# Kernel optimization log

Measured on AMD Instinct MI355X. Metric: run time of the kernel, lower is better.

Reference implementation:

```python
import jax, jax.numpy as jnp
import numpy as np


def _gcn(x, src, dst, W, b, M):
    # GCNConv: out = D^{-1/2} (A+I) D^{-1/2} X W + b, messages flow src->dst
    xw = x @ W  # [M, D]
    loops = jnp.arange(M)
    s = jnp.concatenate([src, loops])
    d = jnp.concatenate([dst, loops])
    deg = jax.ops.segment_sum(jnp.ones_like(s, x.dtype), d, num_segments=M)
    dinv = jnp.where(deg > 0, jax.lax.rsqrt(jnp.maximum(deg, 1.0)), 0.0)
    norm = dinv[s] * dinv[d]  # [Eg+M]
    return jax.ops.segment_sum(norm[:, None] * xw[s], d, num_segments=M) + b


def _graph_cross_attention(values, k, q, e_src, e_dst, N):
    # gather-dot, segment softmax over destination tokens, scatter-sum of values
    scale = jnp.sqrt(jnp.asarray(k.shape[1], k.dtype))
    dots = (q[e_dst] * k[e_src]).sum(-1) / scale  # [Ea]
    m = jax.ops.segment_max(dots, e_dst, num_segments=N)
    m = jnp.where(jnp.isfinite(m), m, 0.0)
    w = jnp.exp(dots - m[e_dst])
    den = jax.ops.segment_sum(w, e_dst, num_segments=N)
    w = w / jnp.where(den > 0, den, 1.0)[e_dst]
    return jax.ops.segment_sum(w[:, None] * values[e_src], e_dst, num_segments=N)


def reference(token_embeddings, tokens2edges, edge_index, e2t_src, e2t_dst,
              W_gnn, b_gnn, Wk, bk, Wq, bq, Wl, bl, gate_a, gate_b):
    N = token_embeddings.shape[1]
    M = tokens2edges.shape[1]

    def per_sample(t, t2e, ei, es, ed):
        edge_emb = t[t2e]                                  # [M, D] gather
        edge_emb = _gcn(edge_emb, ei[0], ei[1], W_gnn, b_gnn, M)
        k = edge_emb @ Wk + bk                             # [M, 64]
        q = t @ Wq + bq                                    # [N, 64]
        gatt = _graph_cross_attention(edge_emb, k, q, es, ed, N)  # [N, D]
        new = t + jnp.tanh(gate_a) * gatt
        new = new + jnp.tanh(gate_b) * (new @ Wl + bl)
        return new

    return jax.vmap(per_sample)(token_embeddings, tokens2edges, edge_index, e2t_src, e2t_dst)


def setup_inputs() -> dict:
    B, N, M, Eg, Ea, D, DK = 4, 4096, 16384, 65536, 65536, 512, 64
    key = jax.random.key(0)
    ks = jax.random.split(key, 16)
    s = 0.05  # weight scale to keep activations well-conditioned
    return {
        "token_embeddings": jax.random.normal(ks[0], (B, N, D), jnp.float32),
        "tokens2edges": jax.random.randint(ks[1], (B, M), 0, N),
        "edge_index": jax.random.randint(ks[2], (B, 2, Eg), 0, M),
        "e2t_src": jax.random.randint(ks[3], (B, Ea), 0, M),
        "e2t_dst": jax.random.randint(ks[4], (B, Ea), 0, N),
        "W_gnn": jax.random.normal(ks[5], (D, D), jnp.float32) * s,
        "b_gnn": jax.random.normal(ks[6], (D,), jnp.float32) * s,
        "Wk": jax.random.normal(ks[7], (D, DK), jnp.float32) * s,
        "bk": jax.random.normal(ks[8], (DK,), jnp.float32) * s,
        "Wq": jax.random.normal(ks[9], (D, DK), jnp.float32) * s,
        "bq": jax.random.normal(ks[10], (DK,), jnp.float32) * s,
        "Wl": jax.random.normal(ks[11], (D, D), jnp.float32) * s,
        "bl": jax.random.normal(ks[12], (D,), jnp.float32) * s,
        "gate_a": jax.random.normal(ks[13], (1,), jnp.float32),
        "gate_b": jax.random.normal(ks[14], (1,), jnp.float32),
    }
```

## Files before the change

kernel.cpp:

```cpp
#include <hip/hip_runtime.h>
#include <math.h>

#define BB 4
#define NT 4096
#define ME 16384
#define EG 65536
#define EA 65536
#define DD 512
#define DKK 64

using bf16x8 = __attribute__((ext_vector_type(8))) short;
using f32x4  = __attribute__((ext_vector_type(4))) float;

static __device__ __forceinline__ unsigned short f2bf(float f) {
    unsigned u = __float_as_uint(f);
    u += 0x7fffu + ((u >> 16) & 1u);
    return (unsigned short)(u >> 16);
}
static __device__ __forceinline__ float bf2f(unsigned short u) {
    return __uint_as_float((unsigned)u << 16);
}
static __device__ __forceinline__ void acc8(float* a, uint4 v, float s) {
    a[0] += s * __uint_as_float(v.x << 16);
    a[1] += s * __uint_as_float(v.x & 0xffff0000u);
    a[2] += s * __uint_as_float(v.y << 16);
    a[3] += s * __uint_as_float(v.y & 0xffff0000u);
    a[4] += s * __uint_as_float(v.z << 16);
    a[5] += s * __uint_as_float(v.z & 0xffff0000u);
    a[6] += s * __uint_as_float(v.w << 16);
    a[7] += s * __uint_as_float(v.w & 0xffff0000u);
}
static __device__ __forceinline__ uint4 pack8(const float* a) {
    uint4 o;
    o.x = (unsigned)f2bf(a[0]) | ((unsigned)f2bf(a[1]) << 16);
    o.y = (unsigned)f2bf(a[2]) | ((unsigned)f2bf(a[3]) << 16);
    o.z = (unsigned)f2bf(a[4]) | ((unsigned)f2bf(a[5]) << 16);
    o.w = (unsigned)f2bf(a[6]) | ((unsigned)f2bf(a[7]) << 16);
    return o;
}

#define PREP_GEMM  8
#define PREP_CAST  (PREP_GEMM + 8192)
#define PREP_TRA   (PREP_CAST + 1024)
#define PREP_WQ    (PREP_TRA + 128)
#define PREP_WLT   (PREP_WQ + 1024)
#define PREP_BIAS  (PREP_WLT + 67)
#define PREP_HIST  (PREP_BIAS + 2048)
__global__ __launch_bounds__(256) void k_prep(
    const float* __restrict__ Wgnn, const float* __restrict__ Wk,
    const float* __restrict__ Wq, const float* __restrict__ Wl,
    const float* __restrict__ bgnn, const float* __restrict__ bk,
    const float* __restrict__ bq, const float* __restrict__ t_all,
    const int* __restrict__ ei_all, const int* __restrict__ ed_all,
    unsigned short* __restrict__ BtT, unsigned short* __restrict__ Wlt,
    float* __restrict__ biasG, float* __restrict__ bias640,
    unsigned short* __restrict__ tb, int* __restrict__ cntG, int* __restrict__ cntA)
{
    __shared__ float smem[2048];
    int bx = blockIdx.x, tid = threadIdx.x;
    if (bx < PREP_GEMM) {
        float (*As)[64] = (float(*)[64])smem;
        float (*Bs)[64] = (float(*)[64])(smem + 1024);
        int tx = tid & 15, ty = tid >> 4;
        int bm = bx * 64;
        float acc[4][4] = {};
        long aoff = (long)(bm + (tid >> 2)) * DD;
        int kk0 = (tid & 3) * 4;
        int arowl = tid >> 2;
        for (int k0 = 0; k0 < DD; k0 += 16) {
            float4 av = *(const float4*)(Wgnn + aoff + k0 + kk0);
            As[kk0 + 0][arowl] = av.x;
            As[kk0 + 1][arowl] = av.y;
            As[kk0 + 2][arowl] = av.z;
            As[kk0 + 3][arowl] = av.w;
            float4 bv = *(const float4*)(Wk + (long)(k0 + ty) * 64 + tx * 4);
            *(float4*)&Bs[ty][tx * 4] = bv;
            __syncthreads();
#pragma unroll
            for (int k = 0; k < 16; ++k) {
                float4 a = *(const float4*)&As[k][ty * 4];
                float4 b = *(const float4*)&Bs[k][tx * 4];
                acc[0][0] += a.x * b.x; acc[0][1] += a.x * b.y; acc[0][2] += a.x * b.z; acc[0][3] += a.x * b.w;
                acc[1][0] += a.y * b.x; acc[1][1] += a.y * b.y; acc[1][2] += a.y * b.z; acc[1][3] += a.y * b.w;
                acc[2][0] += a.z * b.x; acc[2][1] += a.z * b.y; acc[2][2] += a.z * b.z; acc[2][3] += a.z * b.w;
                acc[3][0] += a.w * b.x; acc[3][1] += a.w * b.y; acc[3][2] += a.w * b.z; acc[3][3] += a.w * b.w;
            }
            __syncthreads();
        }
#pragma unroll
        for (int j = 0; j < 4; ++j) {
            int c = tx * 4 + j;
#pragma unroll
            for (int i = 0; i < 4; ++i) {
                int k = bm + ty * 4 + i;
                BtT[(long)(512 + c) * DD + k] = f2bf(acc[i][j]);
            }
        }
    } else if (bx < PREP_CAST) {
        long i = (long)(bx - PREP_GEMM) * 256 + tid;
        float4 v = *(const float4*)(t_all + (i << 2));
        ushort4 o;
        o.x = f2bf(v.x); o.y = f2bf(v.y); o.z = f2bf(v.z); o.w = f2bf(v.w);
        *(ushort4*)(tb + (i << 2)) = o;
    } else if (bx < PREP_TRA) {
        int i = (bx - PREP_CAST) * 256 + tid;
        int n = i >> 9, k = i & 511;
        BtT[i] = f2bf(Wgnn[((long)k << 9) + n]);
    } else if (bx < PREP_WQ) {
        int i = (bx - PREP_TRA) * 256 + tid;
        int n = i >> 9, k = i & 511;
        BtT[(long)(576 + n) * DD + k] = f2bf(Wq[k * 64 + n]);
    } else if (bx < PREP_WLT) {
        int j = (bx - PREP_WQ) * 256 + tid;
        int n = j >> 9, k = j & 511;
        Wlt[j] = f2bf(Wl[((long)k << 9) + n]);
    } else if (bx < PREP_BIAS) {
        int bb = bx - PREP_WLT;
        if (bb < 3) {
            int i = bb * 256 + tid;
            if (i < 512) { biasG[i] = bgnn[i]; bias640[i] = 0.0f; }
            else if (i < 576) { bias640[i] = 0.0f; }
            else if (i < 640) { bias640[i] = bq[i - 576]; }
            return;
        }
        int n = bb - 3;
        float* red = smem;
        float s = 0.0f;
        for (int k = tid; k < DD; k += 256) s += bgnn[k] * Wk[k * 64 + n];
        red[tid] = s;
        __syncthreads();
        for (int d = 128; d > 0; d >>= 1) {
            if (tid < d) red[tid] += red[tid + d];
            __syncthreads();
        }
        if (tid == 0) biasG[512 + n] = red[0] + bk[n];
    } else {
        int i = (bx - PREP_BIAS) * 256 + tid;
        if (i < BB * EG) {
            int b = i >> 16, e = i & (EG - 1);
            int dst = ei_all[(size_t)b * 2 * EG + EG + e];
            atomicAdd(&cntG[b * ME + dst], 1);
        } else {
            int j = i - BB * EG;
            atomicAdd(&cntA[(j >> 16) * NT + ed_all[j]], 1);
        }
    }
}

__global__ __launch_bounds__(1024) void k_scan2(
    const int* __restrict__ cntG, int* __restrict__ offsG, int* __restrict__ curG,
    float* __restrict__ dinv,
    const int* __restrict__ cntA, int* __restrict__ offsA, int* __restrict__ curA) {
    __shared__ int sums[1024];
    int tid = threadIdx.x;
    int bid = blockIdx.x;
    const int* cnt;
    int *offs, *cur;
    float* dv = nullptr;
    int C, nk;
    if (bid < BB) {
        cnt = cntG + bid * ME; offs = offsG + bid * (ME + 1); cur = curG + bid * ME;
        dv = dinv + bid * ME; C = ME / 1024; nk = ME;
    } else {
        int b = bid - BB;
        cnt = cntA + b * NT; offs = offsA + b * (NT + 1); cur = curA + b * NT;
        C = NT / 1024; nk = NT;
    }
    int local[16];
    int tot = 0;
    for (int i = 0; i < C; ++i) { local[i] = cnt[tid * C + i]; tot += local[i]; }
    sums[tid] = tot;
    __syncthreads();
    for (int d = 1; d < 1024; d <<= 1) {
        int v = (tid >= d) ? sums[tid - d] : 0;
        __syncthreads();
        sums[tid] += v;
        __syncthreads();
    }
    int run = sums[tid] - tot;
    for (int i = 0; i < C; ++i) {
        int idx = tid * C + i;
        offs[idx] = run;
        cur[idx] = run;
        if (dv) dv[idx] = rsqrtf((float)local[i] + 1.0f);
        run += local[i];
    }
    if (tid == 1023) offs[nk] = run;
}

__global__ __launch_bounds__(256, 2) void k_fill_token(
    const int* __restrict__ ei_all, const int* __restrict__ es_all,
    const int* __restrict__ ed_all, const int* __restrict__ t2e_all,
    const float* __restrict__ dinv,
    int* __restrict__ curG, int2* __restrict__ csrG,
    int* __restrict__ curA, int2* __restrict__ csrA,
    const unsigned short* __restrict__ A, const unsigned short* __restrict__ BtT,
    const float* __restrict__ bias640, unsigned short* __restrict__ Xg,
    unsigned short* __restrict__ Xk, unsigned short* __restrict__ qmatb)
{
    __shared__ short As[64 * 32];
    __shared__ short Bs[320 * 32];
    int tid = threadIdx.x;
    int bxx = blockIdx.x;

    if (bxx >= 512) {
        int i = (bxx - 512) * 256 + tid;
        if (i < BB * EG) {
            int b = i >> 16, e = i & (EG - 1);
            const int* ei = ei_all + (size_t)b * 2 * EG;
            int s = ei[e], d = ei[EG + e];
            int p = atomicAdd(&curG[b * ME + d], 1);
            int2 v;
            v.x = t2e_all[(b << 14) + s];
            v.y = __float_as_int(dinv[b * ME + s]);
            csrG[(size_t)b * EG + p] = v;
        } else {
            int j = i - BB * EG;
            int b = j >> 16;
            int p = atomicAdd(&curA[b * NT + ed_all[j]], 1);
            int2 v;
            v.x = es_all[j];
            v.y = ed_all[j];
            csrA[(size_t)b * EA + p] = v;
        }
        return;
    }

    int lane = tid & 63;
    int w = tid >> 6;
    long bm = (long)(bxx >> 1) * 64;
    int bcol = (bxx & 1) * 320;
    const unsigned short* Bblk = BtT + (long)bcol * DD;

    f32x4 acc[4][5] = {};

    for (int k0 = 0; k0 < DD; k0 += 32) {
        {
            int s = tid;
            int r = s >> 2;
            int gc = ((s & 3) ^ ((s >> 3) & 3)) * 8;
            __builtin_amdgcn_global_load_lds(
                (const __attribute__((address_space(1))) unsigned int*)(A + (bm + r) * DD + k0 + gc),
                (__attribute__((address_space(3))) unsigned int*)(As + s * 8), 16, 0, 0);
        }
#pragma unroll
        for (int i = 0; i < 5; ++i) {
            int s = tid + i * 256;
            int r = s >> 2;
            int gc = ((s & 3) ^ ((s >> 3) & 3)) * 8;
            __builtin_amdgcn_global_load_lds(
                (const __attribute__((address_space(1))) unsigned int*)(Bblk + (long)r * DD + k0 + gc),
                (__attribute__((address_space(3))) unsigned int*)(Bs + s * 8), 16, 0, 0);
        }
        __syncthreads();

        int cq = lane >> 4;
        bf16x8 af[4];
#pragma unroll
        for (int rb = 0; rb < 4; ++rb) {
            int r = rb * 16 + (lane & 15);
            af[rb] = *(const bf16x8*)&As[(r * 4 + (cq ^ ((r >> 1) & 3))) * 8];
        }
#pragma unroll
        for (int cb = 0; cb < 5; ++cb) {
            int r = w * 80 + cb * 16 + (lane & 15);
            bf16x8 bf = *(const bf16x8*)&Bs[(r * 4 + (cq ^ ((r >> 1) & 3))) * 8];
#pragma unroll
            for (int rb = 0; rb < 4; ++rb)
                acc[rb][cb] = __builtin_amdgcn_mfma_f32_16x16x32_bf16(af[rb], bf, acc[rb][cb], 0, 0, 0);
        }
        __syncthreads();
    }

#pragma unroll
    for (int rb = 0; rb < 4; ++rb) {
        long row0 = bm + rb * 16 + ((lane >> 4) << 2);
#pragma unroll
        for (int cb = 0; cb < 5; ++cb) {
            int col = bcol + w * 80 + cb * 16 + (lane & 15);
            float bv = bias640[col];
            if (col < 512) {
#pragma unroll
                for (int r = 0; r < 4; ++r)
                    Xg[(row0 + r) * DD + col] = f2bf(acc[rb][cb][r] + bv);
            } else if (col < 576) {
#pragma unroll
                for (int r = 0; r < 4; ++r)
                    Xk[(row0 + r) * DKK + (col - 512)] = f2bf(acc[rb][cb][r] + bv);
            } else {
#pragma unroll
                for (int r = 0; r < 4; ++r)
                    qmatb[(row0 + r) * DKK + (col - 576)] = f2bf(acc[rb][cb][r] + bv);
            }
        }
    }
}

__global__ __launch_bounds__(256) void k_gcn_gather(
    const unsigned short* __restrict__ Xg, const unsigned short* __restrict__ Xk,
    const int* __restrict__ t2e_all, const float* __restrict__ dinv,
    const int* __restrict__ offsG, const int2* __restrict__ csrG,
    const float* __restrict__ biasG,
    unsigned short* __restrict__ eeb, unsigned short* __restrict__ kmatb)
{
    int w = threadIdx.x >> 6;
    int lane = threadIdx.x & 63;
    int bx = blockIdx.x;
    int b = (bx & 7) >> 1;
    int half = bx & 1;
    int idx = bx >> 3;
    int m = (half * 2048 + idx) * 4 + w;
    int mg = (b << 14) + m;
    const int* offs = offsG + b * (ME + 1);
    const int2* csr = csrG + (size_t)b * EG;
    const unsigned short* gl = Xg + (((long)b * NT) << 9) + lane * 8;
    const unsigned short* kl = Xk + ((long)b * NT) * DKK + lane;

    float dm = dinv[mg];
    int self = t2e_all[mg];
    uint4 vself = *(const uint4*)(gl + ((long)self << 9));
    float kself = bf2f(kl[(long)self * DKK]);

    float a[8] = {0, 0, 0, 0, 0, 0, 0, 0};
    float ak = 0.0f;
    int p = offs[m], end = offs[m + 1];
    for (; p + 4 <= end; p += 4) {
        int2 e0 = csr[p], e1 = csr[p + 1], e2 = csr[p + 2], e3 = csr[p + 3];
        uint4 r0 = *(const uint4*)(gl + ((long)e0.x << 9));
        uint4 r1 = *(const uint4*)(gl + ((long)e1.x << 9));
        uint4 r2 = *(const uint4*)(gl + ((long)e2.x << 9));
        uint4 r3 = *(const uint4*)(gl + ((long)e3.x << 9));
        float k0 = bf2f(kl[(long)e0.x * DKK]);
        float k1 = bf2f(kl[(long)e1.x * DKK]);
        float k2 = bf2f(kl[(long)e2.x * DKK]);
        float k3 = bf2f(kl[(long)e3.x * DKK]);
        float w0 = __int_as_float(e0.y), w1 = __int_as_float(e1.y);
        float w2 = __int_as_float(e2.y), w3 = __int_as_float(e3.y);
        acc8(a, r0, w0); ak += w0 * k0;
        acc8(a, r1, w1); ak += w1 * k1;
        acc8(a, r2, w2); ak += w2 * k2;
        acc8(a, r3, w3); ak += w3 * k3;
    }
    if (p < end) {
        int e1m = end - 1;
        int i1 = min(p + 1, e1m), i2 = min(p + 2, e1m), i3 = min(p + 3, e1m);
        int2 e0 = csr[p], e1 = csr[i1], e2 = csr[i2], e3 = csr[i3];
        uint4 r0 = *(const uint4*)(gl + ((long)e0.x << 9));
        uint4 r1 = *(const uint4*)(gl + ((long)e1.x << 9));
        uint4 r2 = *(const uint4*)(gl + ((long)e2.x << 9));
        uint4 r3 = *(const uint4*)(gl + ((long)e3.x << 9));
        float k0 = bf2f(kl[(long)e0.x * DKK]);
        float k1 = bf2f(kl[(long)e1.x * DKK]);
        float k2 = bf2f(kl[(long)e2.x * DKK]);
        float k3 = bf2f(kl[(long)e3.x * DKK]);
        float w0 = __int_as_float(e0.y);
        float w1 = (p + 1 < end) ? __int_as_float(e1.y) : 0.0f;
        float w2 = (p + 2 < end) ? __int_as_float(e2.y) : 0.0f;
        float w3 = (p + 3 < end) ? __int_as_float(e3.y) : 0.0f;
        acc8(a, r0, w0); ak += w0 * k0;
        acc8(a, r1, w1); ak += w1 * k1;
        acc8(a, r2, w2); ak += w2 * k2;
        acc8(a, r3, w3); ak += w3 * k3;
    }
    acc8(a, vself, dm);
    ak += dm * kself;

    const float* bg = biasG + lane * 8;
    float4 b0 = *(const float4*)bg;
    float4 b1 = *(const float4*)(bg + 4);
    a[0] = dm * a[0] + b0.x; a[1] = dm * a[1] + b0.y;
    a[2] = dm * a[2] + b0.z; a[3] = dm * a[3] + b0.w;
    a[4] = dm * a[4] + b1.x; a[5] = dm * a[5] + b1.y;
    a[6] = dm * a[6] + b1.z; a[7] = dm * a[7] + b1.w;
    *(uint4*)(eeb + ((long)mg << 9) + lane * 8) = pack8(a);
    kmatb[(long)mg * DKK + lane] = f2bf(dm * ak + biasG[512 + lane]);
}

__global__ void k_dots(const unsigned short* __restrict__ kmatb,
                       const unsigned short* __restrict__ qmatb,
                       const int2* __restrict__ csrA, int2* __restrict__ swbuf) {
    int bx = blockIdx.x;
    int b = (bx & 7) >> 1;
    int half = bx & 1;
    int idx = bx >> 3;
    int p = (b << 16) + (half * 128 + idx) * 256 + threadIdx.x;
    int2 sd = csrA[p];
    const uint4* kr = (const uint4*)(kmatb + ((long)(b * ME + sd.x) << 6));
    const uint4* qr = (const uint4*)(qmatb + ((long)(b * NT + sd.y) << 6));
    float dot = 0.0f;
#pragma unroll
    for (int j = 0; j < 8; ++j) {
        uint4 kv = kr[j];
        uint4 qv = qr[j];
        dot += __uint_as_float(kv.x << 16) * __uint_as_float(qv.x << 16)
             + __uint_as_float(kv.x & 0xffff0000u) * __uint_as_float(qv.x & 0xffff0000u)
             + __uint_as_float(kv.y << 16) * __uint_as_float(qv.y << 16)
             + __uint_as_float(kv.y & 0xffff0000u) * __uint_as_float(qv.y & 0xffff0000u)
             + __uint_as_float(kv.z << 16) * __uint_as_float(qv.z << 16)
             + __uint_as_float(kv.z & 0xffff0000u) * __uint_as_float(qv.z & 0xffff0000u)
             + __uint_as_float(kv.w << 16) * __uint_as_float(qv.w << 16)
             + __uint_as_float(kv.w & 0xffff0000u) * __uint_as_float(qv.w & 0xffff0000u);
    }
    int2 o;
    o.x = sd.x;
    o.y = __float_as_int(expf(dot * 0.125f));
    swbuf[p] = o;
}

__global__ __launch_bounds__(256) void k_att_gather(
    const unsigned short* __restrict__ eeb, const int2* __restrict__ swbuf,
    const int* __restrict__ offsA,
    const float* __restrict__ t_all, const float* __restrict__ ga,
    float* __restrict__ out, unsigned short* __restrict__ nb)
{
    int w = threadIdx.x >> 6;
    int lane = threadIdx.x & 63;
    int bx = blockIdx.x;
    int b = (bx & 7) >> 1;
    int half = bx & 1;
    int idx = bx >> 3;
    int n = (half * 512 + idx) * 4 + w;
    int ng = (b << 12) + n;
    const int* offs = offsA + b * (NT + 1);
    const int2* swb = swbuf + (size_t)b * EA;
    const unsigned short* el = eeb + (((size_t)b * ME) << 9) + lane * 8;

    float a[8] = {0, 0, 0, 0, 0, 0, 0, 0};
    float den = 0.0f;
    int p = offs[n], end = offs[n + 1];
    for (; p + 8 <= end; p += 8) {
        int2 e0 = swb[p],     e1 = swb[p + 1], e2 = swb[p + 2], e3 = swb[p + 3];
        int2 e4 = swb[p + 4], e5 = swb[p + 5], e6 = swb[p + 6], e7 = swb[p + 7];
        uint4 r0 = *(const uint4*)(el + ((long)e0.x << 9));
        uint4 r1 = *(const uint4*)(el + ((long)e1.x << 9));
        uint4 r2 = *(const uint4*)(el + ((long)e2.x << 9));
        uint4 r3 = *(const uint4*)(el + ((long)e3.x << 9));
        uint4 r4 = *(const uint4*)(el + ((long)e4.x << 9));
        uint4 r5 = *(const uint4*)(el + ((long)e5.x << 9));
        uint4 r6 = *(const uint4*)(el + ((long)e6.x << 9));
        uint4 r7 = *(const uint4*)(el + ((long)e7.x << 9));
        float w0 = __int_as_float(e0.y), w1 = __int_as_float(e1.y);
        float w2 = __int_as_float(e2.y), w3 = __int_as_float(e3.y);
        float w4 = __int_as_float(e4.y), w5 = __int_as_float(e5.y);
        float w6 = __int_as_float(e6.y), w7 = __int_as_float(e7.y);
        den += (w0 + w1 + w2 + w3) + (w4 + w5 + w6 + w7);
        acc8(a, r0, w0);
        acc8(a, r1, w1);
        acc8(a, r2, w2);
        acc8(a, r3, w3);
        acc8(a, r4, w4);
        acc8(a, r5, w5);
        acc8(a, r6, w6);
        acc8(a, r7, w7);
    }
    if (p < end) {
        int e1m = end - 1;
        int2 e0 = swb[p];
        int2 e1 = swb[min(p + 1, e1m)];
        int2 e2 = swb[min(p + 2, e1m)];
        int2 e3 = swb[min(p + 3, e1m)];
        int2 e4 = swb[min(p + 4, e1m)];
        int2 e5 = swb[min(p + 5, e1m)];
        int2 e6 = swb[min(p + 6, e1m)];
        int2 e7 = swb[min(p + 7, e1m)];
        uint4 r0 = *(const uint4*)(el + ((long)e0.x << 9));
        uint4 r1 = *(const uint4*)(el + ((long)e1.x << 9));
        uint4 r2 = *(const uint4*)(el + ((long)e2.x << 9));
        uint4 r3 = *(const uint4*)(el + ((long)e3.x << 9));
        uint4 r4 = *(const uint4*)(el + ((long)e4.x << 9));
        uint4 r5 = *(const uint4*)(el + ((long)e5.x << 9));
        uint4 r6 = *(const uint4*)(el + ((long)e6.x << 9));
        uint4 r7 = *(const uint4*)(el + ((long)e7.x << 9));
        float w0 = __int_as_float(e0.y);
        float w1 = (p + 1 < end) ? __int_as_float(e1.y) : 0.0f;
        float w2 = (p + 2 < end) ? __int_as_float(e2.y) : 0.0f;
        float w3 = (p + 3 < end) ? __int_as_float(e3.y) : 0.0f;
        float w4 = (p + 4 < end) ? __int_as_float(e4.y) : 0.0f;
        float w5 = (p + 5 < end) ? __int_as_float(e5.y) : 0.0f;
        float w6 = (p + 6 < end) ? __int_as_float(e6.y) : 0.0f;
        float w7 = (p + 7 < end) ? __int_as_float(e7.y) : 0.0f;
        den += (w0 + w1 + w2 + w3) + (w4 + w5 + w6 + w7);
        acc8(a, r0, w0);
        acc8(a, r1, w1);
        acc8(a, r2, w2);
        acc8(a, r3, w3);
        acc8(a, r4, w4);
        acc8(a, r5, w5);
        acc8(a, r6, w6);
        acc8(a, r7, w7);
    }
    float g = tanhf(ga[0]);
    float inv = den > 0.0f ? g / den : 0.0f;
    const float* tr = t_all + ((long)ng << 9) + lane * 8;
    float4 t0 = *(const float4*)tr;
    float4 t1 = *(const float4*)(tr + 4);
    float o[8];
    o[0] = t0.x + inv * a[0]; o[1] = t0.y + inv * a[1];
    o[2] = t0.z + inv * a[2]; o[3] = t0.w + inv * a[3];
    o[4] = t1.x + inv * a[4]; o[5] = t1.y + inv * a[5];
    o[6] = t1.z + inv * a[6]; o[7] = t1.w + inv * a[7];
    float* op = out + ((long)ng << 9) + lane * 8;
    *(float4*)op = make_float4(o[0], o[1], o[2], o[3]);
    *(float4*)(op + 4) = make_float4(o[4], o[5], o[6], o[7]);
    *(uint4*)(nb + ((long)ng << 9) + lane * 8) = pack8(o);
}

__global__ __launch_bounds__(256, 2) void gemm_final(
    const unsigned short* __restrict__ A, const unsigned short* __restrict__ Bt,
    const float* __restrict__ bias, float* __restrict__ Cf, const float* __restrict__ gs)
{
    constexpr int CB = 8;
    constexpr int BROWS = 2 * CB * 16;
    __shared__ short As[128 * 32];
    __shared__ short Bs[BROWS * 32];
    int tid = threadIdx.x;
    int lane = tid & 63;
    int w = tid >> 6;
    int wm = w >> 1, wn = w & 1;
    long bm = (long)blockIdx.x * 128;
    int bcol = blockIdx.y * BROWS;
    const unsigned short* Bblk = Bt + (long)bcol * DD;

    f32x4 acc[4][CB] = {};

    for (int k0 = 0; k0 < DD; k0 += 32) {
#pragma unroll
        for (int i = 0; i < 2; ++i) {
            int s = tid + i * 256;
            int r = s >> 2;
            int gc = ((s & 3) ^ ((s >> 3) & 3)) * 8;
            __builtin_amdgcn_global_load_lds(
                (const __attribute__((address_space(1))) unsigned int*)(A + (bm + r) * DD + k0 + gc),
                (__attribute__((address_space(3))) unsigned int*)(As + s * 8), 16, 0, 0);
        }
#pragma unroll
        for (int i = 0; i < CB / 2; ++i) {
            int s = tid + i * 256;
            int r = s >> 2;
            int gc = ((s & 3) ^ ((s >> 3) & 3)) * 8;
            __builtin_amdgcn_global_load_lds(
                (const __attribute__((address_space(1))) unsigned int*)(Bblk + (long)r * DD + k0 + gc),
                (__attribute__((address_space(3))) unsigned int*)(Bs + s * 8), 16, 0, 0);
        }
        __syncthreads();

        int cq = lane >> 4;
        bf16x8 af[4];
#pragma unroll
        for (int rb = 0; rb < 4; ++rb) {
            int r = wm * 64 + rb * 16 + (lane & 15);
            af[rb] = *(const bf16x8*)&As[(r * 4 + (cq ^ ((r >> 1) & 3))) * 8];
        }
#pragma unroll
        for (int cb = 0; cb < CB; ++cb) {
            int r = wn * (CB * 16) + cb * 16 + (lane & 15);
            bf16x8 bf = *(const bf16x8*)&Bs[(r * 4 + (cq ^ ((r >> 1) & 3))) * 8];
#pragma unroll
            for (int rb = 0; rb < 4; ++rb)
                acc[rb][cb] = __builtin_amdgcn_mfma_f32_16x16x32_bf16(af[rb], bf, acc[rb][cb], 0, 0, 0);
        }
        __syncthreads();
    }

    float g = tanhf(gs[0]);
#pragma unroll
    for (int rb = 0; rb < 4; ++rb) {
        long row0 = bm + wm * 64 + rb * 16 + ((lane >> 4) << 2);
#pragma unroll
        for (int cb = 0; cb < CB; ++cb) {
            int col = bcol + wn * (CB * 16) + cb * 16 + (lane & 15);
            float bv = bias[col];
#pragma unroll
            for (int r = 0; r < 4; ++r)
                Cf[(row0 + r) * DD + col] += g * (acc[rb][cb][r] + bv);
        }
    }
}

extern "C" void kernel_launch(void* const* d_in, const int* in_sizes, int n_in,
                              void* d_out, int out_size, void* d_ws, size_t ws_size,
                              hipStream_t stream) {
    const float* t_all   = (const float*)d_in[0];
    const int*   t2e_all = (const int*)d_in[1];
    const int*   ei_all  = (const int*)d_in[2];
    const int*   es_all  = (const int*)d_in[3];
    const int*   ed_all  = (const int*)d_in[4];
    const float* Wgnn    = (const float*)d_in[5];
    const float* bgnn    = (const float*)d_in[6];
    const float* Wk      = (const float*)d_in[7];
    const float* bk      = (const float*)d_in[8];
    const float* Wq      = (const float*)d_in[9];
    const float* bq      = (const float*)d_in[10];
    const float* Wl      = (const float*)d_in[11];
    const float* bl      = (const float*)d_in[12];
    const float* ga      = (const float*)d_in[13];
    const float* gb      = (const float*)d_in[14];
    float* out = (float*)d_out;

    char* wsb = (char*)d_ws;
    size_t off = 0;
    unsigned short* eeb   = (unsigned short*)(wsb + off); off += (size_t)BB * ME * DD * 2;
    unsigned short* tb    = (unsigned short*)(wsb + off); off += (size_t)BB * NT * DD * 2;
    unsigned short* Xg    = (unsigned short*)(wsb + off); off += (size_t)BB * NT * DD * 2;
    unsigned short* nb    = (unsigned short*)(wsb + off); off += (size_t)BB * NT * DD * 2;
    unsigned short* Xk    = (unsigned short*)(wsb + off); off += (size_t)BB * NT * DKK * 2;
    unsigned short* qmatb = (unsigned short*)(wsb + off); off += (size_t)BB * NT * DKK * 2;
    unsigned short* kmatb = (unsigned short*)(wsb + off); off += (size_t)BB * ME * DKK * 2;
    unsigned short* BtT   = (unsigned short*)(wsb + off); off += (size_t)640 * DD * 2;
    unsigned short* Wlt   = (unsigned short*)(wsb + off); off += (size_t)DD * DD * 2;
    float* biasG   = (float*)(wsb + off); off += 576 * 4;
    float* bias640 = (float*)(wsb + off); off += 640 * 4;
    float* dinv  = (float*)(wsb + off); off += (size_t)BB * ME * 4;
    int2* swbuf  = (int2*)(wsb + off); off += (size_t)BB * EA * 8;
    int* cntG  = (int*)(wsb + off); off += (size_t)BB * ME * 4;
    int* cntA  = (int*)(wsb + off); off += (size_t)BB * NT * 4;
    int* offsG = (int*)(wsb + off); off += (size_t)BB * (ME + 1) * 4;
    int* curG  = (int*)(wsb + off); off += (size_t)BB * ME * 4;
    int2* csrG = (int2*)(wsb + off); off += (size_t)BB * EG * 8;
    int* offsA = (int*)(wsb + off); off += (size_t)BB * (NT + 1) * 4;
    int* curA  = (int*)(wsb + off); off += (size_t)BB * NT * 4;
    int2* csrA = (int2*)(wsb + off); off += (size_t)BB * EA * 8;

    hipMemsetAsync(cntG, 0, (size_t)BB * (ME + NT) * 4, stream);
    k_prep<<<PREP_HIST, 256, 0, stream>>>(
        Wgnn, Wk, Wq, Wl, bgnn, bk, bq, t_all, ei_all, ed_all,
        BtT, Wlt, biasG, bias640, tb, cntG, cntA);

    k_scan2<<<2 * BB, 1024, 0, stream>>>(cntG, offsG, curG, dinv, cntA, offsA, curA);

    k_fill_token<<<512 + 2048, 256, 0, stream>>>(
        ei_all, es_all, ed_all, t2e_all, dinv, curG, csrG, curA, csrA,
        tb, BtT, bias640, Xg, Xk, qmatb);

    k_gcn_gather<<<(BB * ME * 64) / 256, 256, 0, stream>>>(
        Xg, Xk, t2e_all, dinv, offsG, csrG, biasG, eeb, kmatb);

    k_dots<<<(BB * EA) / 256, 256, 0, stream>>>(kmatb, qmatb, csrA, swbuf);
    k_att_gather<<<(BB * NT * 64) / 256, 256, 0, stream>>>(
        eeb, swbuf, offsA, t_all, ga, out, nb);

    gemm_final<<<dim3((BB * NT) / 128, 2), 256, 0, stream>>>(nb, Wlt, bl, out, gb);
}
```

Before: 339.8 us.

## Refuse prep, scan, CSR fill and token GEMM stages into new kernel boundaries

Histogram blocks now come first in the prep kernel. The CSR offset scan is merged into the token projection GEMM kernel, whose 1024-thread blocks leave only 256 threads active for the GEMM. The GCN CSR fill gets its own kernel, and the attention CSR fill is folded into the GCN gather kernel as extra leading blocks. The aim is to overlap the small serial scan and fill work with heavier GEMM and gather work, but the 1024-thread GEMM blocks with mostly idle threads and larger LDS use may reduce occupancy.

Result: no change. 346.2 us (+1.9%).

```diff
diff --git a/kernel.cpp b/kernel.cpp
--- a/kernel.cpp
+++ b/kernel.cpp
@@ -39,13 +39,13 @@
     return o;
 }
 
-#define PREP_GEMM  8
-#define PREP_CAST  (PREP_GEMM + 8192)
-#define PREP_TRA   (PREP_CAST + 1024)
-#define PREP_WQ    (PREP_TRA + 128)
-#define PREP_WLT   (PREP_WQ + 1024)
-#define PREP_BIAS  (PREP_WLT + 67)
-#define PREP_HIST  (PREP_BIAS + 2048)
+#define P_HIST 2048
+#define P_CAST (P_HIST + 8192)
+#define P_MG   (P_CAST + 8)
+#define P_TRA  (P_MG + 1024)
+#define P_WQ   (P_TRA + 128)
+#define P_WLT  (P_WQ + 1024)
+#define P_BIAS (P_WLT + 67)
 __global__ __launch_bounds__(256) void k_prep(
     const float* __restrict__ Wgnn, const float* __restrict__ Wk,
     const float* __restrict__ Wq, const float* __restrict__ Wl,
@@ -58,11 +58,27 @@
 {
     __shared__ float smem[2048];
     int bx = blockIdx.x, tid = threadIdx.x;
-    if (bx < PREP_GEMM) {
+    if (bx < P_HIST) {
+        int i = bx * 256 + tid;
+        if (i < BB * EG) {
+            int b = i >> 16, e = i & (EG - 1);
+            int dst = ei_all[(size_t)b * 2 * EG + EG + e];
+            atomicAdd(&cntG[b * ME + dst], 1);
+        } else {
+            int j = i - BB * EG;
+            atomicAdd(&cntA[(j >> 16) * NT + ed_all[j]], 1);
+        }
+    } else if (bx < P_CAST) {
+        long i = (long)(bx - P_HIST) * 256 + tid;
+        float4 v = *(const float4*)(t_all + (i << 2));
+        ushort4 o;
+        o.x = f2bf(v.x); o.y = f2bf(v.y); o.z = f2bf(v.z); o.w = f2bf(v.w);
+        *(ushort4*)(tb + (i << 2)) = o;
+    } else if (bx < P_MG) {
         float (*As)[64] = (float(*)[64])smem;
         float (*Bs)[64] = (float(*)[64])(smem + 1024);
         int tx = tid & 15, ty = tid >> 4;
-        int bm = bx * 64;
+        int bm = (bx - P_CAST) * 64;
         float acc[4][4] = {};
         long aoff = (long)(bm + (tid >> 2)) * DD;
         int kk0 = (tid & 3) * 4;
@@ -96,26 +112,20 @@
                 BtT[(long)(512 + c) * DD + k] = f2bf(acc[i][j]);
             }
         }
-    } else if (bx < PREP_CAST) {
-        long i = (long)(bx - PREP_GEMM) * 256 + tid;
-        float4 v = *(const float4*)(t_all + (i << 2));
-        ushort4 o;
-        o.x = f2bf(v.x); o.y = f2bf(v.y); o.z = f2bf(v.z); o.w = f2bf(v.w);
-        *(ushort4*)(tb + (i << 2)) = o;
-    } else if (bx < PREP_TRA) {
-        int i = (bx - PREP_CAST) * 256 + tid;
+    } else if (bx < P_TRA) {
+        int i = (bx - P_MG) * 256 + tid;
         int n = i >> 9, k = i & 511;
         BtT[i] = f2bf(Wgnn[((long)k << 9) + n]);
-    } else if (bx < PREP_WQ) {
-        int i = (bx - PREP_TRA) * 256 + tid;
+    } else if (bx < P_WQ) {
+        int i = (bx - P_TRA) * 256 + tid;
         int n = i >> 9, k = i & 511;
         BtT[(long)(576 + n) * DD + k] = f2bf(Wq[k * 64 + n]);
-    } else if (bx < PREP_WLT) {
-        int j = (bx - PREP_WQ) * 256 + tid;
+    } else if (bx < P_WLT) {
+        int j = (bx - P_WQ) * 256 + tid;
         int n = j >> 9, k = j & 511;
         Wlt[j] = f2bf(Wl[((long)k << 9) + n]);
-    } else if (bx < PREP_BIAS) {
-        int bb = bx - PREP_WLT;
+    } else {
+        int bb = bx - P_WLT;
         if (bb < 3) {
             int i = bb * 256 + tid;
             if (i < 512) { biasG[i] = bgnn[i]; bias640[i] = 0.0f; }
@@ -134,166 +144,148 @@
             __syncthreads();
         }
         if (tid == 0) biasG[512 + n] = red[0] + bk[n];
-    } else {
-        int i = (bx - PREP_BIAS) * 256 + tid;
-        if (i < BB * EG) {
-            int b = i >> 16, e = i & (EG - 1);
-            int dst = ei_all[(size_t)b * 2 * EG + EG + e];
-            atomicAdd(&cntG[b * ME + dst], 1);
-        } else {
-            int j = i - BB * EG;
-            atomicAdd(&cntA[(j >> 16) * NT + ed_all[j]], 1);
-        }
-    }
-}
-
-__global__ __launch_bounds__(1024) void k_scan2(
+    }
+}
+
+__global__ __launch_bounds__(1024) void k_scan_token(
     const int* __restrict__ cntG, int* __restrict__ offsG, int* __restrict__ curG,
     float* __restrict__ dinv,
-    const int* __restrict__ cntA, int* __restrict__ offsA, int* __restrict__ curA) {
-    __shared__ int sums[1024];
-    int tid = threadIdx.x;
-    int bid = blockIdx.x;
-    const int* cnt;
-    int *offs, *cur;
-    float* dv = nullptr;
-    int C, nk;
-    if (bid < BB) {
-        cnt = cntG + bid * ME; offs = offsG + bid * (ME + 1); cur = curG + bid * ME;
-        dv = dinv + bid * ME; C = ME / 1024; nk = ME;
-    } else {
-        int b = bid - BB;
-        cnt = cntA + b * NT; offs = offsA + b * (NT + 1); cur = curA + b * NT;
-        C = NT / 1024; nk = NT;
-    }
-    int local[16];
-    int tot = 0;
-    for (int i = 0; i < C; ++i) { local[i] = cnt[tid * C + i]; tot += local[i]; }
-    sums[tid] = tot;
-    __syncthreads();
-    for (int d = 1; d < 1024; d <<= 1) {
-        int v = (tid >= d) ? sums[tid - d] : 0;
-        __syncthreads();
-        sums[tid] += v;
-        __syncthreads();
-    }
-    int run = sums[tid] - tot;
-    for (int i = 0; i < C; ++i) {
-        int idx = tid * C + i;
-        offs[idx] = run;
-        cur[idx] = run;
-        if (dv) dv[idx] = rsqrtf((float)local[i] + 1.0f);
-        run += local[i];
-    }
-    if (tid == 1023) offs[nk] = run;
-}
-
-__global__ __launch_bounds__(256, 2) void k_fill_token(
-    const int* __restrict__ ei_all, const int* __restrict__ es_all,
-    const int* __restrict__ ed_all, const int* __restrict__ t2e_all,
-    const float* __restrict__ dinv,
-    int* __restrict__ curG, int2* __restrict__ csrG,
-    int* __restrict__ curA, int2* __restrict__ csrA,
+    const int* __restrict__ cntA, int* __restrict__ offsA, int* __restrict__ curA,
     const unsigned short* __restrict__ A, const unsigned short* __restrict__ BtT,
     const float* __restrict__ bias640, unsigned short* __restrict__ Xg,
     unsigned short* __restrict__ Xk, unsigned short* __restrict__ qmatb)
 {
+    __shared__ int sums[1024];
     __shared__ short As[64 * 32];
     __shared__ short Bs[320 * 32];
     int tid = threadIdx.x;
-    int bxx = blockIdx.x;
-
-    if (bxx >= 512) {
-        int i = (bxx - 512) * 256 + tid;
-        if (i < BB * EG) {
-            int b = i >> 16, e = i & (EG - 1);
-            const int* ei = ei_all + (size_t)b * 2 * EG;
-            int s = ei[e], d = ei[EG + e];
-            int p = atomicAdd(&curG[b * ME + d], 1);
-            int2 v;
-            v.x = t2e_all[(b << 14) + s];
-            v.y = __float_as_int(dinv[b * ME + s]);
-            csrG[(size_t)b * EG + p] = v;
+    int bid = blockIdx.x;
+
+    if (bid < 2 * BB) {
+        const int* cnt;
+        int *offs, *cur;
+        float* dv = nullptr;
+        int C, nk;
+        if (bid < BB) {
+            cnt = cntG + bid * ME; offs = offsG + bid * (ME + 1); cur = curG + bid * ME;
+            dv = dinv + bid * ME; C = ME / 1024; nk = ME;
         } else {
-            int j = i - BB * EG;
-            int b = j >> 16;
-            int p = atomicAdd(&curA[b * NT + ed_all[j]], 1);
-            int2 v;
-            v.x = es_all[j];
-            v.y = ed_all[j];
-            csrA[(size_t)b * EA + p] = v;
-        }
+            int b = bid - BB;
+            cnt = cntA + b * NT; offs = offsA + b * (NT + 1); cur = curA + b * NT;
+            C = NT / 1024; nk = NT;
+        }
+        int local[16];
+        int tot = 0;
+        for (int i = 0; i < C; ++i) { local[i] = cnt[tid * C + i]; tot += local[i]; }
+        sums[tid] = tot;
+        __syncthreads();
+        for (int d = 1; d < 1024; d <<= 1) {
+            int v = (tid >= d) ? sums[tid - d] : 0;
+            __syncthreads();
+            sums[tid] += v;
+            __syncthreads();
+        }
+        int run = sums[tid] - tot;
+        for (int i = 0; i < C; ++i) {
+            int idx = tid * C + i;
+            offs[idx] = run;
+            cur[idx] = run;
+            if (dv) dv[idx] = rsqrtf((float)local[i] + 1.0f);
+            run += local[i];
+        }
+        if (tid == 1023) offs[nk] = run;
         return;
     }
 
+    int g = bid - 2 * BB;
+    bool act = tid < 256;
     int lane = tid & 63;
-    int w = tid >> 6;
-    long bm = (long)(bxx >> 1) * 64;
-    int bcol = (bxx & 1) * 320;
+    int w = (tid >> 6) & 3;
+    long bm = (long)(g >> 1) * 64;
+    int bcol = (g & 1) * 320;
     const unsigned short* Bblk = BtT + (long)bcol * DD;
 
     f32x4 acc[4][5] = {};
 
     for (int k0 = 0; k0 < DD; k0 += 32) {
-        {
-            int s = tid;
-            int r = s >> 2;
-            int gc = ((s & 3) ^ ((s >> 3) & 3)) * 8;
-            __builtin_amdgcn_global_load_lds(
-                (const __attribute__((address_space(1))) unsigned int*)(A + (bm + r) * DD + k0 + gc),
-                (__attribute__((address_space(3))) unsigned int*)(As + s * 8), 16, 0, 0);
-        }
-#pragma unroll
-        for (int i = 0; i < 5; ++i) {
-            int s = tid + i * 256;
-            int r = s >> 2;
-            int gc = ((s & 3) ^ ((s >> 3) & 3)) * 8;
-            __builtin_amdgcn_global_load_lds(
-                (const __attribute__((address_space(1))) unsigned int*)(Bblk + (long)r * DD + k0 + gc),
-                (__attribute__((address_space(3))) unsigned int*)(Bs + s * 8), 16, 0, 0);
+        if (act) {
+            {
+                int s = tid;
+                int r = s >> 2;
+                int gc = ((s & 3) ^ ((s >> 3) & 3)) * 8;
+                __builtin_amdgcn_global_load_lds(
+                    (const __attribute__((address_space(1))) unsigned int*)(A + (bm + r) * DD + k0 + gc),
+                    (__attribute__((address_space(3))) unsigned int*)(As + s * 8), 16, 0, 0);
+            }
+#pragma unroll
+            for (int i = 0; i < 5; ++i) {
+                int s = tid + i * 256;
+                int r = s >> 2;
+                int gc = ((s & 3) ^ ((s >> 3) & 3)) * 8;
+                __builtin_amdgcn_global_load_lds(
+                    (const __attribute__((address_space(1))) unsigned int*)(Bblk + (long)r * DD + k0 + gc),
+                    (__attribute__((address_space(3))) unsigned int*)(Bs + s * 8), 16, 0, 0);
+            }
         }
         __syncthreads();
-
-        int cq = lane >> 4;
-        bf16x8 af[4];
+        if (act) {
+            int cq = lane >> 4;
+            bf16x8 af[4];
+#pragma unroll
+            for (int rb = 0; rb < 4; ++rb) {
+                int r = rb * 16 + (lane & 15);
+                af[rb] = *(const bf16x8*)&As[(r * 4 + (cq ^ ((r >> 1) & 3))) * 8];
+            }
+#pragma unroll
+            for (int cb = 0; cb < 5; ++cb) {
+                int r = w * 80 + cb * 16 + (lane & 15);
+                bf16x8 bf = *(const bf16x8*)&Bs[(r * 4 + (cq ^ ((r >> 1) & 3))) * 8];
+#pragma unroll
+                for (int rb = 0; rb < 4; ++rb)
+                    acc[rb][cb] = __builtin_amdgcn_mfma_f32_16x16x32_bf16(af[rb], bf, acc[rb][cb], 0, 0, 0);
+            }
+        }
+        __syncthreads();
+    }
+
+    if (act) {
 #pragma unroll
         for (int rb = 0; rb < 4; ++rb) {
-            int r = rb * 16 + (lane & 15);
-            af[rb] = *(const bf16x8*)&As[(r * 4 + (cq ^ ((r >> 1) & 3))) * 8];
-        }
-#pragma unroll
-        for (int cb = 0; cb < 5; ++cb) {
-            int r = w * 80 + cb * 16 + (lane & 15);
-            bf16x8 bf = *(const bf16x8*)&Bs[(r * 4 + (cq ^ ((r >> 1) & 3))) * 8];
-#pragma unroll
-            for (int rb = 0; rb < 4; ++rb)
-                acc[rb][cb] = __builtin_amdgcn_mfma_f32_16x16x32_bf16(af[rb], bf, acc[rb][cb], 0, 0, 0);
-        }
-        __syncthreads();
-    }
-
-#pragma unroll
-    for (int rb = 0; rb < 4; ++rb) {
-        long row0 = bm + rb * 16 + ((lane >> 4) << 2);
-#pragma unroll
-        for (int cb = 0; cb < 5; ++cb) {
-            int col = bcol + w * 80 + cb * 16 + (lane & 15);
-            float bv = bias640[col];
-            if (col < 512) {
-#pragma unroll
-                for (int r = 0; r < 4; ++r)
-                    Xg[(row0 + r) * DD + col] = f2bf(acc[rb][cb][r] + bv);
-            } else if (col < 576) {
-#pragma unroll
-                for (int r = 0; r < 4; ++r)
-                    Xk[(row0 + r) * DKK + (col - 512)] = f2bf(acc[rb][cb][r] + bv);
-            } else {
-#pragma unroll
-                for (int r = 0; r < 4; ++r)
-                    qmatb[(row0 + r) * DKK + (col - 576)] = f2bf(acc[rb][cb][r] + bv);
+            long row0 = bm + rb * 16 + ((lane >> 4) << 2);
+#pragma unroll
+            for (int cb = 0; cb < 5; ++cb) {
+                int col = bcol + w * 80 + cb * 16 + (lane & 15);
+                float bv = bias640[col];
+                if (col < 512) {
+#pragma unroll
+                    for (int r = 0; r < 4; ++r)
+                        Xg[(row0 + r) * DD + col] = f2bf(acc[rb][cb][r] + bv);
+                } else if (col < 576) {
+#pragma unroll
+                    for (int r = 0; r < 4; ++r)
+                        Xk[(row0 + r) * DKK + (col - 512)] = f2bf(acc[rb][cb][r] + bv);
+                } else {
+#pragma unroll
+                    for (int r = 0; r < 4; ++r)
+                        qmatb[(row0 + r) * DKK + (col - 576)] = f2bf(acc[rb][cb][r] + bv);
+                }
             }
         }
     }
+}
+
+__global__ void k_fillg(const int* __restrict__ ei_all, const int* __restrict__ t2e_all,
+                        const float* __restrict__ dinv,
+                        int* __restrict__ curG, int2* __restrict__ csrG) {
+    int i = blockIdx.x * 256 + threadIdx.x;
+    int b = i >> 16, e = i & (EG - 1);
+    const int* ei = ei_all + (size_t)b * 2 * EG;
+    int s = ei[e], d = ei[EG + e];
+    int p = atomicAdd(&curG[b * ME + d], 1);
+    int2 v;
+    v.x = t2e_all[(b << 14) + s];
+    v.y = __float_as_int(dinv[b * ME + s]);
+    csrG[(size_t)b * EG + p] = v;
 }
 
 __global__ __launch_bounds__(256) void k_gcn_gather(
@@ -301,11 +293,24 @@
     const int* __restrict__ t2e_all, const float* __restrict__ dinv,
     const int* __restrict__ offsG, const int2* __restrict__ csrG,
     const float* __restrict__ biasG,
-    unsigned short* __restrict__ eeb, unsigned short* __restrict__ kmatb)
+    unsigned short* __restrict__ eeb, unsigned short* __restrict__ kmatb,
+    const int* __restrict__ es_all, const int* __restrict__ ed_all,
+    int* __restrict__ curA, int2* __restrict__ csrA)
 {
-    int w = threadIdx.x >> 6;
-    int lane = threadIdx.x & 63;
-    int bx = blockIdx.x;
+    int tid = threadIdx.x;
+    if (blockIdx.x < 1024) {
+        int j = blockIdx.x * 256 + tid;
+        int b = j >> 16;
+        int p = atomicAdd(&curA[b * NT + ed_all[j]], 1);
+        int2 v;
+        v.x = es_all[j];
+        v.y = ed_all[j];
+        csrA[(size_t)b * EA + p] = v;
+        return;
+    }
+    int w = tid >> 6;
+    int lane = tid & 63;
+    int bx = blockIdx.x - 1024;
     int b = (bx & 7) >> 1;
     int half = bx & 1;
     int idx = bx >> 3;
@@ -622,18 +627,19 @@
     int2* csrA = (int2*)(wsb + off); off += (size_t)BB * EA * 8;
 
     hipMemsetAsync(cntG, 0, (size_t)BB * (ME + NT) * 4, stream);
-    k_prep<<<PREP_HIST, 256, 0, stream>>>(
+    k_prep<<<P_BIAS, 256, 0, stream>>>(
         Wgnn, Wk, Wq, Wl, bgnn, bk, bq, t_all, ei_all, ed_all,
         BtT, Wlt, biasG, bias640, tb, cntG, cntA);
 
-    k_scan2<<<2 * BB, 1024, 0, stream>>>(cntG, offsG, curG, dinv, cntA, offsA, curA);
-
-    k_fill_token<<<512 + 2048, 256, 0, stream>>>(
-        ei_all, es_all, ed_all, t2e_all, dinv, curG, csrG, curA, csrA,
+    k_scan_token<<<2 * BB + 512, 1024, 0, stream>>>(
+        cntG, offsG, curG, dinv, cntA, offsA, curA,
         tb, BtT, bias640, Xg, Xk, qmatb);
 
-    k_gcn_gather<<<(BB * ME * 64) / 256, 256, 0, stream>>>(
-        Xg, Xk, t2e_all, dinv, offsG, csrG, biasG, eeb, kmatb);
+    k_fillg<<<(BB * EG) / 256, 256, 0, stream>>>(ei_all, t2e_all, dinv, curG, csrG);
+
+    k_gcn_gather<<<1024 + (BB * ME * 64) / 256, 256, 0, stream>>>(
+        Xg, Xk, t2e_all, dinv, offsG, csrG, biasG, eeb, kmatb,
+        es_all, ed_all, curA, csrA);
 
     k_dots<<<(BB * EA) / 256, 256, 0, stream>>>(kmatb, qmatb, csrA, swbuf);
     k_att_gather<<<(BB * NT * 64) / 256, 256, 0, stream>>>(
```
